# Optimization experiments

Measured on AMD Instinct MI355X. Metric: run time of the kernel, lower is better.

The kernel has to match this reference:

```python
import jax, jax.numpy as jnp
import numpy as np

B, T, DM, H, D = 4, 2048, 1024, 16, 64
INNER = H * D


def setup_inputs() -> dict:
    key = jax.random.key(0)
    ks = jax.random.split(key, 8)
    s = 0.02
    x = jax.random.normal(ks[0], (B, T, DM), dtype=jnp.float32)
    state = jnp.zeros((B, H, D, D), dtype=jnp.float32)
    Wq = jax.random.normal(ks[1], (DM, INNER), dtype=jnp.float32) * s
    Wk = jax.random.normal(ks[2], (DM, INNER), dtype=jnp.float32) * s
    Wv = jax.random.normal(ks[3], (DM, INNER), dtype=jnp.float32) * s
    Wa = jax.random.normal(ks[4], (DM, H), dtype=jnp.float32) * s
    ba = jnp.zeros((H,), dtype=jnp.float32)
    Wb = jax.random.normal(ks[5], (DM, H), dtype=jnp.float32) * s
    bb = jnp.zeros((H,), dtype=jnp.float32)  # beta_init=0.5 -> logit(0.5)=0
    Wo = jax.random.normal(ks[6], (INNER, DM), dtype=jnp.float32) * s
    return {"x": x, "state": state, "Wq": Wq, "Wk": Wk, "Wv": Wv,
            "Wa": Wa, "ba": ba, "Wb": Wb, "bb": bb, "Wo": Wo}


def reference(x, state, Wq, Wk, Wv, Wa, ba, Wb, bb, Wo):
    Bb, Tt, _ = x.shape
    Q = (x @ Wq).reshape(Bb, Tt, H, D)
    K = (x @ Wk).reshape(Bb, Tt, H, D)
    V = (x @ Wv).reshape(Bb, Tt, H, D)
    alpha = jax.nn.sigmoid(x @ Wa + ba)  # (B,T,H) forget gate
    beta = jax.nn.sigmoid(x @ Wb + bb)   # (B,T,H) write gate
    # F.normalize(p=2, dim=-1) with eps=1e-12 clamp on the norm
    K = K / jnp.maximum(jnp.linalg.norm(K, axis=-1, keepdims=True), 1e-12)

    def step(S, inp):
        qt, kt, vt, at, bt = inp  # (B,H,D),(B,H,D),(B,H,D),(B,H),(B,H)
        S = at[..., None, None] * S + bt[..., None, None] * jnp.einsum('bhi,bhj->bhij', vt, kt)
        yt = jnp.einsum('bhij,bhj->bhi', S, qt)
        return S, yt

    xs = (jnp.swapaxes(Q, 0, 1), jnp.swapaxes(K, 0, 1), jnp.swapaxes(V, 0, 1),
          jnp.swapaxes(alpha, 0, 1), jnp.swapaxes(beta, 0, 1))
    S, ys = jax.lax.scan(step, state, xs)  # ys: (T,B,H,D)
    out = jnp.swapaxes(ys, 0, 1).reshape(Bb, Tt, INNER) @ Wo
    return out, S
```

## Files before the change

kernel.cpp:

```cpp
#include <hip/hip_runtime.h>
#include <hip/hip_bf16.h>
#include <math.h>

#define B_SZ   4
#define T_LEN  2048
#define DM     1024
#define NH     16
#define DH     64
#define INNER  1024
#define NROWS  (B_SZ*T_LEN)
#define NQ     (NROWS*INNER)
#define CH     64
#define NCH    (T_LEN/CH)

typedef __bf16 bf16x8 __attribute__((ext_vector_type(8)));
typedef __bf16 bf16x4 __attribute__((ext_vector_type(4)));
typedef float  f32x4  __attribute__((ext_vector_type(4)));
typedef __attribute__((address_space(3))) void*       lds_vp;
typedef const __attribute__((address_space(1))) void* gbl_vp;

__device__ __forceinline__ int swz(int row, int col) {
    return (row << 6) + ((((col >> 3) + (row >> 2)) & 7) << 3) + (col & 7);
}

__global__ __launch_bounds__(256) void wt_cast_transpose(const float* __restrict__ Wq,
                                                         const float* __restrict__ Wk,
                                                         const float* __restrict__ Wv,
                                                         const float* __restrict__ Wo,
                                                         __bf16* __restrict__ WqT,
                                                         __bf16* __restrict__ WkT,
                                                         __bf16* __restrict__ WvT,
                                                         __bf16* __restrict__ WoT) {
    __shared__ float tile[64][65];
    const float* W;
    __bf16* WT;
    if      (blockIdx.z == 0) { W = Wq; WT = WqT; }
    else if (blockIdx.z == 1) { W = Wk; WT = WkT; }
    else if (blockIdx.z == 2) { W = Wv; WT = WvT; }
    else                      { W = Wo; WT = WoT; }

    const int k0 = blockIdx.y * 64, n0 = blockIdx.x * 64;
    const int tr  = threadIdx.x >> 4;
    const int tc4 = (threadIdx.x & 15) * 4;

#pragma unroll
    for (int r = 0; r < 4; r++) {
        const int k = tr + 16 * r;
        const float4 v = *(const float4*)(W + (size_t)(k0 + k) * DM + n0 + tc4);
        tile[k][tc4 + 0] = v.x;
        tile[k][tc4 + 1] = v.y;
        tile[k][tc4 + 2] = v.z;
        tile[k][tc4 + 3] = v.w;
    }
    __syncthreads();
#pragma unroll
    for (int r = 0; r < 4; r++) {
        const int n = tr + 16 * r;
        bf16x4 o;
#pragma unroll
        for (int j = 0; j < 4; j++) o[j] = (__bf16)tile[tc4 + j][n];
        *(bf16x4*)(WT + (size_t)(n0 + n) * DM + k0 + tc4) = o;
    }
}

#define A_LOFF(buf_, kh_) ((buf_) * 32768 + (kh_) * 16384)
#define B_LOFF(buf_, kh_) (65536 + (buf_) * 16384 + (kh_) * 8192)

template <typename CT>
__device__ __forceinline__ void gemm_8ph_body(const __bf16* __restrict__ A,
                                              const __bf16* __restrict__ BT,
                                              CT* __restrict__ C,
                                              int m0, int n0bt, int n0c) {
    __shared__ __align__(16) char lds[98304];

    const int tid  = threadIdx.x;
    const int wid  = tid >> 6;
    const int lane = tid & 63;
    const int wm = wid >> 1;
    const int wn = wid & 1;
    const int frow = lane & 15, quad = lane >> 4;

    int offA[4], offB[4];
#pragma unroll
    for (int i = 0; i < 4; ++i) {
        const int ra = wm * 64 + i * 16 + frow;
        offA[i] = ra * 64 + ((quad ^ ((ra >> 1) & 3)) << 4);
        const int rb = wn * 64 + i * 16 + frow;
        offB[i] = rb * 64 + ((quad ^ ((rb >> 1) & 3)) << 4);
    }

    const int lr = lane >> 2;
    const int cs = ((lane & 3) ^ ((lane >> 3) & 3)) << 3;
    const __bf16* gA0 = A  + (size_t)(m0 + (wid * 2 + 0) * 16 + lr) * 1024 + cs;
    const __bf16* gA1 = A  + (size_t)(m0 + (wid * 2 + 1) * 16 + lr) * 1024 + cs;
    const __bf16* gB  = BT + (size_t)(n0bt + wid * 16 + lr) * 1024 + cs;

#define STG_A(t_, kh_) do {                                                        \
        __builtin_amdgcn_global_load_lds((gbl_vp)(gA0 + (t_) * 64 + (kh_) * 32),   \
            (lds_vp)(lds + A_LOFF((t_) & 1, kh_) + (wid * 2 + 0) * 1024), 16, 0, 0); \
        __builtin_amdgcn_global_load_lds((gbl_vp)(gA1 + (t_) * 64 + (kh_) * 32),   \
            (lds_vp)(lds + A_LOFF((t_) & 1, kh_) + (wid * 2 + 1) * 1024), 16, 0, 0); \
    } while (0)
#define STG_B(t_, kh_)                                                             \
        __builtin_amdgcn_global_load_lds((gbl_vp)(gB + (t_) * 64 + (kh_) * 32),    \
            (lds_vp)(lds + B_LOFF((t_) & 1, kh_) + wid * 1024), 16, 0, 0)

    f32x4 acc[4][4];
#pragma unroll
    for (int i = 0; i < 4; i++)
#pragma unroll
        for (int j = 0; j < 4; j++) acc[i][j] = (f32x4)0.f;

    STG_A(0, 0); STG_A(0, 1); STG_B(0, 0); STG_B(0, 1);
    STG_A(1, 0); STG_B(1, 0);
    asm volatile("s_waitcnt vmcnt(3)" ::: "memory");
    asm volatile("s_barrier" ::: "memory");

#define PHASE(u_, kh_, STG_STMT, VM_STMT)                                          \
    {                                                                              \
        const char* Ab_ = lds + A_LOFF((u_) & 1, kh_);                             \
        const char* Bb_ = lds + B_LOFF((u_) & 1, kh_);                             \
        bf16x8 af_[4], bfr_[4];                                                    \
        _Pragma("unroll")                                                          \
        for (int i_ = 0; i_ < 4; ++i_) {                                           \
            af_[i_]  = *(const bf16x8*)(Ab_ + offA[i_]);                           \
            bfr_[i_] = *(const bf16x8*)(Bb_ + offB[i_]);                           \
        }                                                                          \
        STG_STMT;                                                                  \
        asm volatile("s_barrier" ::: "memory");                                    \
        asm volatile("s_waitcnt lgkmcnt(0)" ::: "memory");                         \
        __builtin_amdgcn_sched_barrier(0);                                         \
        __builtin_amdgcn_s_setprio(1);                                             \
        _Pragma("unroll")                                                          \
        for (int mi_ = 0; mi_ < 4; ++mi_)                                          \
            _Pragma("unroll")                                                      \
            for (int nj_ = 0; nj_ < 4; ++nj_)                                      \
                acc[mi_][nj_] = __builtin_amdgcn_mfma_f32_16x16x32_bf16(           \
                    af_[mi_], bfr_[nj_], acc[mi_][nj_], 0, 0, 0);                  \
        __builtin_amdgcn_s_setprio(0);                                             \
        VM_STMT;                                                                   \
        asm volatile("s_barrier" ::: "memory");                                    \
    }

    for (int u = 0; u < 14; ++u) {
        PHASE(u, 0, { STG_A(u + 1, 1); STG_B(u + 1, 1); }, );
        PHASE(u, 1, { STG_A(u + 2, 0); STG_B(u + 2, 0); },
              asm volatile("s_waitcnt vmcnt(3)" ::: "memory"));
    }
    PHASE(14, 0, { STG_A(15, 1); STG_B(15, 1); }, );
    PHASE(14, 1, { }, asm volatile("s_waitcnt vmcnt(0)" ::: "memory"));
    PHASE(15, 0, { }, );
    PHASE(15, 1, { }, );

#undef PHASE
#undef STG_A
#undef STG_B

    const int cr = quad * 4, cc = frow;
#pragma unroll
    for (int mi = 0; mi < 4; ++mi) {
#pragma unroll
        for (int nj = 0; nj < 4; ++nj) {
            CT* Cp = C + (size_t)(m0 + wm * 64 + mi * 16 + cr) * 1024
                       + n0c + wn * 64 + nj * 16 + cc;
#pragma unroll
            for (int r = 0; r < 4; r++) Cp[(size_t)r * 1024] = (CT)acc[mi][nj][r];
        }
    }
}

__global__ __launch_bounds__(512, 2) void qkv_gemm_8ph(const __bf16* __restrict__ xb,
                                                       const __bf16* __restrict__ BTall,
                                                       __bf16* __restrict__ QKV) {
    const int id = blockIdx.x;
    const int wg = (id & 7) * 96 + (id >> 3);
    const int mt = wg / 24, nt = wg % 24;
    const int mat = nt >> 3;
    gemm_8ph_body<__bf16>(xb, BTall, QKV + (size_t)mat * NQ,
                          mt * 256, nt * 128, (nt & 7) * 128);
}

__global__ __launch_bounds__(512, 2) void out_gemm_8ph(const __bf16* __restrict__ Yb,
                                                       const __bf16* __restrict__ WoT,
                                                       float* __restrict__ Cout) {
    const int id = blockIdx.x;
    const int wg = (id & 7) * 32 + (id >> 3);
    const int mt = wg >> 3, nt = wg & 7;
    gemm_8ph_body<float>(Yb, WoT, Cout, mt * 256, nt * 128, nt * 128);
}

#define WGS 1032
#define LAS 40
__global__ __launch_bounds__(256) void gates_fused(const float* __restrict__ x,
                                                   const float* __restrict__ Wa,
                                                   const float* __restrict__ ba,
                                                   const float* __restrict__ Wb,
                                                   const float* __restrict__ bb,
                                                   float* __restrict__ AlphaT,
                                                   float* __restrict__ BetaT,
                                                   __bf16* __restrict__ xb) {
    __shared__ __align__(16) __bf16 lWg[32 * WGS];
    __shared__ __align__(16) __bf16 lA[64 * LAS];

    const int tid = threadIdx.x;
    const int wid = tid >> 6, lane = tid & 63;
    const int quad = lane >> 4, frow = lane & 15;
    const int m0 = blockIdx.x * 64;

    {
        const int kbase = tid * 4;
#pragma unroll
        for (int j = 0; j < 4; j++) {
            const int k = kbase + j;
            const float4* war = (const float4*)(Wa + (size_t)k * NH);
            const float4* wbr = (const float4*)(Wb + (size_t)k * NH);
#pragma unroll
            for (int q = 0; q < 4; q++) {
                const float4 a = war[q], bq = wbr[q];
                lWg[(q * 4 + 0) * WGS + k] = (__bf16)a.x;
                lWg[(q * 4 + 1) * WGS + k] = (__bf16)a.y;
                lWg[(q * 4 + 2) * WGS + k] = (__bf16)a.z;
                lWg[(q * 4 + 3) * WGS + k] = (__bf16)a.w;
                lWg[(16 + q * 4 + 0) * WGS + k] = (__bf16)bq.x;
                lWg[(16 + q * 4 + 1) * WGS + k] = (__bf16)bq.y;
                lWg[(16 + q * 4 + 2) * WGS + k] = (__bf16)bq.z;
                lWg[(16 + q * 4 + 3) * WGS + k] = (__bf16)bq.w;
            }
        }
    }
    const float bias_a = ba[frow];
    const float bias_b = bb[frow];

    const int rrow = tid >> 2;
    const int rk   = (tid & 3) * 8;
    const float* xrow = x + (size_t)(m0 + rrow) * DM + rk;
    float4 c0 = *(const float4*)(xrow + 0);
    float4 c1 = *(const float4*)(xrow + 4);

    f32x4 acc[2];
    acc[0] = (f32x4)0.f; acc[1] = (f32x4)0.f;

    for (int k0 = 0; k0 < DM; k0 += 32) {
        __syncthreads();
        bf16x8 xv;
        xv[0] = (__bf16)c0.x; xv[1] = (__bf16)c0.y; xv[2] = (__bf16)c0.z; xv[3] = (__bf16)c0.w;
        xv[4] = (__bf16)c1.x; xv[5] = (__bf16)c1.y; xv[6] = (__bf16)c1.z; xv[7] = (__bf16)c1.w;
        *(bf16x8*)&lA[rrow * LAS + rk] = xv;
        *(bf16x8*)(xb + (size_t)(m0 + rrow) * DM + k0 + rk) = xv;
        if (k0 + 32 < DM) {
            c0 = *(const float4*)(xrow + k0 + 32);
            c1 = *(const float4*)(xrow + k0 + 36);
        }
        __syncthreads();
        const bf16x8 af = *(const bf16x8*)&lA[(wid * 16 + frow) * LAS + quad * 8];
#pragma unroll
        for (int ct = 0; ct < 2; ct++) {
            const bf16x8 bf = *(const bf16x8*)&lWg[(ct * 16 + frow) * WGS + k0 + quad * 8];
            acc[ct] = __builtin_amdgcn_mfma_f32_16x16x32_bf16(af, bf, acc[ct], 0, 0, 0);
        }
    }

#pragma unroll
    for (int ct = 0; ct < 2; ct++) {
        const float bias = (ct == 0) ? bias_a : bias_b;
        float* dst = (ct == 0) ? AlphaT : BetaT;
#pragma unroll
        for (int r = 0; r < 4; r++) {
            const int row = m0 + wid * 16 + quad * 4 + r;
            const float s = acc[ct][r] + bias;
            dst[(size_t)frow * NROWS + row] = 1.f / (1.f + __expf(-s));
        }
    }
}

__global__ __launch_bounds__(256) void chunk_ds(const __bf16* __restrict__ Q,
                                                const __bf16* __restrict__ K,
                                                __bf16* __restrict__ V,
                                                const float* __restrict__ AlphaT,
                                                const float* __restrict__ BetaT,
                                                float* __restrict__ Dec,
                                                float* __restrict__ DS,
                                                float* __restrict__ ExpT) {
    __shared__ __align__(16) __bf16 Qb[64 * 64];
    __shared__ __align__(16) __bf16 Kb[64 * 64];
    __shared__ __align__(16) __bf16 KTs[64 * 64];
    __shared__ __align__(16) __bf16 VTb[64 * 64];
    __shared__ __align__(16) __bf16 Ab[64 * 64];
    __shared__ float sla[64], sb[64], swd[64];

    const int blk = blockIdx.x;
    const int c = blk & 31, h = (blk >> 5) & 15, b = blk >> 9;
    const int t0 = c * CH;
    const int tid = threadIdx.x;
    const int wid = tid >> 6, lane = tid & 63;
    const size_t rowbase = ((size_t)(b * T_LEN + t0) * NH + h) * DH;

    const int srow = tid >> 3;
    const int scol = (tid & 7) * 8;
    bf16x8 q8[2], k8[2], v8[2];
#pragma unroll
    for (int r = 0; r < 2; r++) {
        const size_t g = rowbase + (size_t)(srow + 32 * r) * INNER + scol;
        q8[r] = *(const bf16x8*)(Q + g);
        k8[r] = *(const bf16x8*)(K + g);
        v8[r] = *(const bf16x8*)(V + g);
    }

    if (tid < 64) {
        const int t = tid;
        const size_t gaT = (size_t)h * NROWS + b * T_LEN + t0 + t;
        const float a  = AlphaT[gaT];
        const float bt = BetaT[gaT];
        float xx = logf(a);
#pragma unroll
        for (int off = 1; off < 64; off <<= 1) {
            const float y = __shfl_up(xx, off, 64);
            if (t >= off) xx += y;
        }
        const float la63 = __shfl(xx, 63, 64);
        sla[t] = xx;
        sb[t]  = bt;
        swd[t] = bt * __expf(la63 - xx);
        ExpT[gaT] = __expf(xx);
        if (t == 63) Dec[(size_t)(b * NH + h) * NCH + c] = __expf(la63);
    }
    __syncthreads();

#pragma unroll
    for (int r = 0; r < 2; r++) {
        const int row = srow + 32 * r;
        float kf[8];
        float ss = 0.f;
#pragma unroll
        for (int j = 0; j < 8; j++) { kf[j] = (float)k8[r][j]; ss += kf[j] * kf[j]; }
        ss += __shfl_xor(ss, 1, 64);
        ss += __shfl_xor(ss, 2, 64);
        ss += __shfl_xor(ss, 4, 64);
        const float scale = 1.f / fmaxf(sqrtf(ss), 1e-12f);
        const float w = swd[row];
        bf16x8 kn8;
#pragma unroll
        for (int j = 0; j < 8; j++) {
            const float kn = kf[j] * scale;
            kn8[j] = (__bf16)kn;
            KTs[swz(scol + j, row)] = (__bf16)(w * kn);
            VTb[swz(scol + j, row)] = v8[r][j];
        }
        *(bf16x8*)&Qb[swz(row, scol)] = q8[r];
        *(bf16x8*)&Kb[swz(row, scol)] = kn8;
    }
    __syncthreads();

    const int quad = lane >> 4;
    const int frow = lane & 15;
    const int tw = wid * 16;

    f32x4 accG[4];
#pragma unroll
    for (int i = 0; i < 4; i++) accG[i] = (f32x4)0.f;
#pragma unroll
    for (int ks = 0; ks < 2; ks++) {
        const int ko = quad * 8 + 32 * ks;
        const bf16x8 aq = *(const bf16x8*)&Qb[swz(tw + frow, ko)];
#pragma unroll
        for (int st = 0; st < 4; st++) {
            const bf16x8 bk = *(const bf16x8*)&Kb[swz(st * 16 + frow, ko)];
            accG[st] = __builtin_amdgcn_mfma_f32_16x16x32_bf16(aq, bk, accG[st], 0, 0, 0);
        }
    }
#pragma unroll
    for (int st = 0; st < 4; st++) {
#pragma unroll
        for (int r = 0; r < 4; r++) {
            const int t = tw + quad * 4 + r;
            const int s = st * 16 + frow;
            const float av = (s <= t) ? __expf(sla[t] - sla[s]) * sb[s] * accG[st][r] : 0.f;
            Ab[swz(t, s)] = (__bf16)av;
        }
    }
    __syncthreads();

    f32x4 accY[4], accD[4];
#pragma unroll
    for (int i = 0; i < 4; i++) { accY[i] = (f32x4)0.f; accD[i] = (f32x4)0.f; }
#pragma unroll
    for (int ks = 0; ks < 2; ks++) {
        const int ko = quad * 8 + 32 * ks;
        const bf16x8 aA = *(const bf16x8*)&Ab[swz(tw + frow, ko)];
        const bf16x8 aV = *(const bf16x8*)&VTb[swz(tw + frow, ko)];
#pragma unroll
        for (int jt = 0; jt < 4; jt++) {
            const bf16x8 bv = *(const bf16x8*)&VTb[swz(jt * 16 + frow, ko)];
            const bf16x8 bk = *(const bf16x8*)&KTs[swz(jt * 16 + frow, ko)];
            accY[jt] = __builtin_amdgcn_mfma_f32_16x16x32_bf16(aA, bv, accY[jt], 0, 0, 0);
            accD[jt] = __builtin_amdgcn_mfma_f32_16x16x32_bf16(aV, bk, accD[jt], 0, 0, 0);
        }
    }
#pragma unroll
    for (int jt = 0; jt < 4; jt++) {
#pragma unroll
        for (int r = 0; r < 4; r++) {
            const int row = tw + quad * 4 + r;
            const size_t g = rowbase + (size_t)row * INNER + jt * 16 + frow;
            V[g]  = (__bf16)accY[jt][r];
            DS[g] = accD[jt][r];
        }
    }
}

__global__ __launch_bounds__(256) void chunk_state(const float* __restrict__ DS,
                                                   const float* __restrict__ Dec,
                                                   const float* __restrict__ state_in,
                                                   float* __restrict__ state_out,
                                                   __bf16* __restrict__ ScB) {
    const int blk = blockIdx.x;
    const int b = blk >> 4, h = blk & 15;
    const int tid = threadIdx.x;
    const int w = tid >> 6;
    const int l = tid & 63;

    float S[16];
    {
        const float* st = state_in + ((size_t)(b * NH + h) * DH + l) * DH + 16 * w;
#pragma unroll
        for (int j4 = 0; j4 < 4; j4++)
            *(float4*)&S[4 * j4] = *(const float4*)(st + 4 * j4);
    }

    for (int c = 0; c < NCH; c++) {
        const int t0 = c * CH;
        const float decay = Dec[(size_t)(b * NH + h) * NCH + c];
        const size_t off = ((size_t)(b * T_LEN + t0 + l) * NH + h) * DH + 16 * w;
        const float* ds = DS + off;
        __bf16* sc = ScB + off;
        float4 dv[4];
#pragma unroll
        for (int j4 = 0; j4 < 4; j4++) dv[j4] = *(const float4*)(ds + 4 * j4);
#pragma unroll
        for (int j4 = 0; j4 < 4; j4++) {
            bf16x4 o;
            o[0] = (__bf16)S[4 * j4 + 0]; o[1] = (__bf16)S[4 * j4 + 1];
            o[2] = (__bf16)S[4 * j4 + 2]; o[3] = (__bf16)S[4 * j4 + 3];
            *(bf16x4*)(sc + 4 * j4) = o;
        }
#pragma unroll
        for (int j4 = 0; j4 < 4; j4++) {
            S[4 * j4 + 0] = decay * S[4 * j4 + 0] + dv[j4].x;
            S[4 * j4 + 1] = decay * S[4 * j4 + 1] + dv[j4].y;
            S[4 * j4 + 2] = decay * S[4 * j4 + 2] + dv[j4].z;
            S[4 * j4 + 3] = decay * S[4 * j4 + 3] + dv[j4].w;
        }
    }

    float* so = state_out + ((size_t)(b * NH + h) * DH + l) * DH + 16 * w;
#pragma unroll
    for (int j4 = 0; j4 < 4; j4++)
        *(float4*)(so + 4 * j4) = *(const float4*)&S[4 * j4];
}

__global__ __launch_bounds__(256) void chunk_y(const __bf16* __restrict__ Q,
                                               const __bf16* __restrict__ ScB,
                                               __bf16* __restrict__ Yb,
                                               const float* __restrict__ ExpT) {
    __shared__ __align__(16) __bf16 Qb[64 * 64];
    __shared__ __align__(16) __bf16 Scb[64 * 64];
    __shared__ float sexp[64];

    const int blk = blockIdx.x;
    const int c = blk & 31, h = (blk >> 5) & 15, b = blk >> 9;
    const int t0 = c * CH;
    const int tid = threadIdx.x;
    const int wid = tid >> 6, lane = tid & 63;
    const size_t rowbase = ((size_t)(b * T_LEN + t0) * NH + h) * DH;

    const int srow = tid >> 3;
    const int scol = (tid & 7) * 8;
    bf16x8 q8[2], s8[2];
#pragma unroll
    for (int r = 0; r < 2; r++) {
        const size_t g = rowbase + (size_t)(srow + 32 * r) * INNER + scol;
        q8[r] = *(const bf16x8*)(Q + g);
        s8[r] = *(const bf16x8*)(ScB + g);
    }

    if (tid < 64)
        sexp[tid] = ExpT[(size_t)h * NROWS + b * T_LEN + t0 + tid];

#pragma unroll
    for (int r = 0; r < 2; r++) {
        *(bf16x8*)&Qb[swz(srow + 32 * r, scol)]  = q8[r];
        *(bf16x8*)&Scb[swz(srow + 32 * r, scol)] = s8[r];
    }
    __syncthreads();

    const int quad = lane >> 4;
    const int frow = lane & 15;
    const int tw = wid * 16;

    f32x4 accU[4];
#pragma unroll
    for (int i = 0; i < 4; i++) accU[i] = (f32x4)0.f;
#pragma unroll
    for (int ks = 0; ks < 2; ks++) {
        const int ko = quad * 8 + 32 * ks;
        const bf16x8 aq = *(const bf16x8*)&Qb[swz(tw + frow, ko)];
#pragma unroll
        for (int it = 0; it < 4; it++) {
            const bf16x8 bs = *(const bf16x8*)&Scb[swz(it * 16 + frow, ko)];
            accU[it] = __builtin_amdgcn_mfma_f32_16x16x32_bf16(aq, bs, accU[it], 0, 0, 0);
        }
    }

#pragma unroll
    for (int it = 0; it < 4; it++) {
#pragma unroll
        for (int r = 0; r < 4; r++) {
            const int t = tw + quad * 4 + r;
            const size_t g = rowbase + (size_t)t * INNER + it * 16 + frow;
            Yb[g] = (__bf16)(sexp[t] * accU[it][r] + (float)Yb[g]);
        }
    }
}

extern "C" void kernel_launch(void* const* d_in, const int* in_sizes, int n_in,
                              void* d_out, int out_size, void* d_ws, size_t ws_size,
                              hipStream_t stream) {
    const float* x     = (const float*)d_in[0];
    const float* state = (const float*)d_in[1];
    const float* Wq    = (const float*)d_in[2];
    const float* Wk    = (const float*)d_in[3];
    const float* Wv    = (const float*)d_in[4];
    const float* Wa    = (const float*)d_in[5];
    const float* ba    = (const float*)d_in[6];
    const float* Wb    = (const float*)d_in[7];
    const float* bb    = (const float*)d_in[8];
    const float* Wo    = (const float*)d_in[9];

    __bf16* Qb    = (__bf16*)d_ws;
    __bf16* Kbf   = Qb + (size_t)NQ;
    __bf16* Vbf   = Kbf + (size_t)NQ;
    float*  DS    = (float*)(Vbf + (size_t)NQ);
    float*  AlphaT= DS + (size_t)NQ;
    float*  BetaT = AlphaT + (size_t)NROWS * NH;
    float*  ExpT  = BetaT + (size_t)NROWS * NH;
    float*  Dec   = ExpT + (size_t)NROWS * NH;
    __bf16* xb    = (__bf16*)(Dec + (size_t)B_SZ * NH * NCH);
    __bf16* ScB   = xb;
    __bf16* WqT   = xb + (size_t)NQ;
    __bf16* WkT   = WqT + (size_t)DM * INNER;
    __bf16* WvT   = WkT + (size_t)DM * INNER;
    __bf16* WoT   = WvT + (size_t)DM * INNER;

    float* out  = (float*)d_out;
    float* Sout = out + (size_t)NQ;

    wt_cast_transpose<<<dim3(16, 16, 4), 256, 0, stream>>>(Wq, Wk, Wv, Wo,
                                                           WqT, WkT, WvT, WoT);
    gates_fused<<<NROWS / 64, 256, 0, stream>>>(x, Wa, ba, Wb, bb,
                                                AlphaT, BetaT, xb);
    qkv_gemm_8ph<<<768, 512, 0, stream>>>(xb, WqT, Qb);
    chunk_ds<<<B_SZ * NH * NCH, 256, 0, stream>>>(Qb, Kbf, Vbf, AlphaT, BetaT,
                                                  Dec, DS, ExpT);
    chunk_state<<<B_SZ * NH, 256, 0, stream>>>(DS, Dec, state, Sout, ScB);
    chunk_y<<<B_SZ * NH * NCH, 256, 0, stream>>>(Qb, ScB, Vbf, ExpT);
    out_gemm_8ph<<<256, 512, 0, stream>>>(Vbf, WoT, out);
}
```

Measured before the change: 292.2 us.

## Triple-buffer LDS in bf16 GEMM to deepen global-load prefetch

Grows the GEMM's LDS staging from two to three k-tile buffers (144 KB). Global-to-LDS loads now run two tiles ahead instead of one, with vmcnt waits relaxed to match. The aim is to hide global memory latency behind MFMA work in the QKV and output projections. The larger LDS footprint caps residency at one block per CU, but the previous 96 KB already did that.

```diff
diff --git a/kernel.cpp b/kernel.cpp
--- a/kernel.cpp
+++ b/kernel.cpp
@@ -63,15 +63,15 @@
     }
 }
 
-#define A_LOFF(buf_, kh_) ((buf_) * 32768 + (kh_) * 16384)
-#define B_LOFF(buf_, kh_) (65536 + (buf_) * 16384 + (kh_) * 8192)
+#define AOF(b_, kh_) ((b_) * 32768 + (kh_) * 16384)
+#define BOF(b_, kh_) (98304 + (b_) * 16384 + (kh_) * 8192)
 
 template <typename CT>
 __device__ __forceinline__ void gemm_8ph_body(const __bf16* __restrict__ A,
                                               const __bf16* __restrict__ BT,
                                               CT* __restrict__ C,
                                               int m0, int n0bt, int n0c) {
-    __shared__ __align__(16) char lds[98304];
+    __shared__ __align__(16) char lds[147456];
 
     const int tid  = threadIdx.x;
     const int wid  = tid >> 6;
@@ -95,15 +95,19 @@
     const __bf16* gA1 = A  + (size_t)(m0 + (wid * 2 + 1) * 16 + lr) * 1024 + cs;
     const __bf16* gB  = BT + (size_t)(n0bt + wid * 16 + lr) * 1024 + cs;
 
-#define STG_A(t_, kh_) do {                                                        \
-        __builtin_amdgcn_global_load_lds((gbl_vp)(gA0 + (t_) * 64 + (kh_) * 32),   \
-            (lds_vp)(lds + A_LOFF((t_) & 1, kh_) + (wid * 2 + 0) * 1024), 16, 0, 0); \
-        __builtin_amdgcn_global_load_lds((gbl_vp)(gA1 + (t_) * 64 + (kh_) * 32),   \
-            (lds_vp)(lds + A_LOFF((t_) & 1, kh_) + (wid * 2 + 1) * 1024), 16, 0, 0); \
+#define STG3(t_, kh_, b_) do {                                                     \
+        __builtin_amdgcn_global_load_lds((gbl_vp)(gA0 + (size_t)(t_) * 64 + (kh_) * 32), \
+            (lds_vp)(lds + AOF(b_, kh_) + (wid * 2 + 0) * 1024), 16, 0, 0);        \
+        __builtin_amdgcn_global_load_lds((gbl_vp)(gA1 + (size_t)(t_) * 64 + (kh_) * 32), \
+            (lds_vp)(lds + AOF(b_, kh_) + (wid * 2 + 1) * 1024), 16, 0, 0);        \
+        __builtin_amdgcn_global_load_lds((gbl_vp)(gB  + (size_t)(t_) * 64 + (kh_) * 32), \
+            (lds_vp)(lds + BOF(b_, kh_) + wid * 1024), 16, 0, 0);                  \
     } while (0)
-#define STG_B(t_, kh_)                                                             \
-        __builtin_amdgcn_global_load_lds((gbl_vp)(gB + (t_) * 64 + (kh_) * 32),    \
-            (lds_vp)(lds + B_LOFF((t_) & 1, kh_) + wid * 1024), 16, 0, 0)
+
+#define VM9 asm volatile("s_waitcnt vmcnt(9)" ::: "memory")
+#define VM6 asm volatile("s_waitcnt vmcnt(6)" ::: "memory")
+#define VM3 asm volatile("s_waitcnt vmcnt(3)" ::: "memory")
+#define VM0 asm volatile("s_waitcnt vmcnt(0)" ::: "memory")
 
     f32x4 acc[4][4];
 #pragma unroll
@@ -111,15 +115,14 @@
 #pragma unroll
         for (int j = 0; j < 4; j++) acc[i][j] = (f32x4)0.f;
 
-    STG_A(0, 0); STG_A(0, 1); STG_B(0, 0); STG_B(0, 1);
-    STG_A(1, 0); STG_B(1, 0);
-    asm volatile("s_waitcnt vmcnt(3)" ::: "memory");
+    STG3(0, 0, 0); STG3(0, 1, 0); STG3(1, 0, 1); STG3(1, 1, 1);
+    VM9;
     asm volatile("s_barrier" ::: "memory");
 
-#define PHASE(u_, kh_, STG_STMT, VM_STMT)                                          \
+#define PH(b_, kh_, STG_STMT, VM_STMT)                                             \
     {                                                                              \
-        const char* Ab_ = lds + A_LOFF((u_) & 1, kh_);                             \
-        const char* Bb_ = lds + B_LOFF((u_) & 1, kh_);                             \
+        const char* Ab_ = lds + AOF(b_, kh_);                                      \
+        const char* Bb_ = lds + BOF(b_, kh_);                                      \
         bf16x8 af_[4], bfr_[4];                                                    \
         _Pragma("unroll")                                                          \
         for (int i_ = 0; i_ < 4; ++i_) {                                           \
@@ -142,19 +145,22 @@
         asm volatile("s_barrier" ::: "memory");                                    \
     }
 
-    for (int u = 0; u < 14; ++u) {
-        PHASE(u, 0, { STG_A(u + 1, 1); STG_B(u + 1, 1); }, );
-        PHASE(u, 1, { STG_A(u + 2, 0); STG_B(u + 2, 0); },
-              asm volatile("s_waitcnt vmcnt(3)" ::: "memory"));
-    }
-    PHASE(14, 0, { STG_A(15, 1); STG_B(15, 1); }, );
-    PHASE(14, 1, { }, asm volatile("s_waitcnt vmcnt(0)" ::: "memory"));
-    PHASE(15, 0, { }, );
-    PHASE(15, 1, { }, );
-
-#undef PHASE
-#undef STG_A
-#undef STG_B
+    for (int u = 0; u < 12; u += 3) {
+        PH(0, 0, STG3(u + 2, 0, 2), VM9);  PH(0, 1, STG3(u + 2, 1, 2), VM9);
+        PH(1, 0, STG3(u + 3, 0, 0), VM9);  PH(1, 1, STG3(u + 3, 1, 0), VM9);
+        PH(2, 0, STG3(u + 4, 0, 1), VM9);  PH(2, 1, STG3(u + 4, 1, 1), VM9);
+    }
+    PH(0, 0, STG3(14, 0, 2), VM9);  PH(0, 1, STG3(14, 1, 2), VM9);
+    PH(1, 0, STG3(15, 0, 0), VM9);  PH(1, 1, STG3(15, 1, 0), VM9);
+    PH(2, 0, , VM6);                PH(2, 1, , VM3);
+    PH(0, 0, , VM0);                PH(0, 1, , );
+
+#undef PH
+#undef STG3
+#undef VM9
+#undef VM6
+#undef VM3
+#undef VM0
 
     const int cr = quad * 4, cc = frow;
 #pragma unroll
```

After: 287.0 us. No clear change (-1.8%).
